# Optimization experiments

Hardware: AMD Instinct MI355X
Metric: run time of the kernel (lower is better)

## Reference

```python
import jax, jax.numpy as jnp
import numpy as np
import math

B, C_IN, S, E, H, DFF = 8, 16, 1024, 128, 8, 512
DH = E // H
EPS_BN = 1e-5
EPS_LN = 1e-5


def _tape_pe(d_model, seq_len):
    pos = jnp.arange(seq_len, dtype=jnp.float32)[:, None]
    div = jnp.exp(jnp.arange(0, d_model, 2, dtype=jnp.float32) * (-math.log(10000.0) / d_model))
    ang = pos * div * (d_model / seq_len)
    pe = jnp.zeros((seq_len, d_model), dtype=jnp.float32)
    pe = pe.at[:, 0::2].set(jnp.sin(ang))
    pe = pe.at[:, 1::2].set(jnp.cos(ang))
    return pe  # [S, E]


def _ln(x, g, b, eps=EPS_LN):
    m = jnp.mean(x, axis=-1, keepdims=True)
    v = jnp.mean((x - m) ** 2, axis=-1, keepdims=True)
    return (x - m) / jnp.sqrt(v + eps) * g + b


def _bn(x, g, b, mean, var, eps=EPS_BN):
    # eval-mode BatchNorm2d over channel axis 1 of NCHW
    sh = (1, -1, 1, 1)
    return (x - mean.reshape(sh)) / jnp.sqrt(var.reshape(sh) + eps) * g.reshape(sh) + b.reshape(sh)


def setup_inputs() -> dict:
    key = jax.random.key(0)
    ks = jax.random.split(key, 24)
    f = lambda k, shape, s=0.05: (jax.random.normal(k, shape, dtype=jnp.float32) * s)
    inp = {
        'x': jax.random.normal(ks[0], (B, C_IN, S), dtype=jnp.float32),
        'conv1_w': f(ks[1], (E * 4, 1, 1, 7)),
        'conv1_b': f(ks[2], (E * 4,)),
        'bn1_g': 1.0 + f(ks[3], (E * 4,)),
        'bn1_b': f(ks[4], (E * 4,)),
        'bn1_m': jnp.zeros((E * 4,), jnp.float32),
        'bn1_v': jnp.ones((E * 4,), jnp.float32),
        'conv2_w': f(ks[5], (E, E * 4, C_IN, 1)),
        'conv2_b': f(ks[6], (E,)),
        'bn2_g': 1.0 + f(ks[7], (E,)),
        'bn2_b': f(ks[8], (E,)),
        'bn2_m': jnp.zeros((E,), jnp.float32),
        'bn2_v': jnp.ones((E,), jnp.float32),
        'wq': f(ks[9], (E, E)),
        'wk': f(ks[10], (E, E)),
        'wv': f(ks[11], (E, E)),
        'rel_bias_table': f(ks[12], (2 * S - 1, H), 0.02),
        'ln_attn_g': jnp.ones((E,), jnp.float32),
        'ln_attn_b': jnp.zeros((E,), jnp.float32),
        'ln1_g': jnp.ones((E,), jnp.float32),
        'ln1_b': jnp.zeros((E,), jnp.float32),
        'ln2_g': jnp.ones((E,), jnp.float32),
        'ln2_b': jnp.zeros((E,), jnp.float32),
        'ff_w1': f(ks[13], (DFF, E)),
        'ff_b1': f(ks[14], (DFF,)),
        'ff_w2': f(ks[15], (E, DFF)),
        'ff_b2': f(ks[16], (E,)),
    }
    return inp


def reference(x, conv1_w, conv1_b, bn1_g, bn1_b, bn1_m, bn1_v,
              conv2_w, conv2_b, bn2_g, bn2_b, bn2_m, bn2_v,
              wq, wk, wv, rel_bias_table,
              ln_attn_g, ln_attn_b, ln1_g, ln1_b, ln2_g, ln2_b,
              ff_w1, ff_b1, ff_w2, ff_b2):
    dn = ('NCHW', 'OIHW', 'NCHW')
    # conv stem: x [B, C_in, S] -> [B, 1, C_in, S]
    h = x[:, None, :, :]
    h = jax.lax.conv_general_dilated(h, conv1_w, (1, 1), [(0, 0), (3, 3)], dimension_numbers=dn)
    h = h + conv1_b[None, :, None, None]
    h = jax.nn.gelu(_bn(h, bn1_g, bn1_b, bn1_m, bn1_v), approximate=False)
    h = jax.lax.conv_general_dilated(h, conv2_w, (1, 1), [(0, 0), (0, 0)], dimension_numbers=dn)
    h = h + conv2_b[None, :, None, None]
    h = jax.nn.gelu(_bn(h, bn2_g, bn2_b, bn2_m, bn2_v), approximate=False)
    x_src = jnp.transpose(h[:, :, 0, :], (0, 2, 1))  # [B, S, E]

    # tAPE absolute positional encoding
    x_pos = x_src + _tape_pe(E, S)[None]

    # Attention_Rel_Scl (eRPE): bias added AFTER softmax, as in the original
    scale = E ** (-0.5)
    q = jnp.einsum('bsd,ed->bse', x_pos, wq).reshape(B, S, H, DH).transpose(0, 2, 1, 3)
    k = jnp.einsum('bsd,ed->bse', x_pos, wk).reshape(B, S, H, DH).transpose(0, 2, 1, 3)
    v = jnp.einsum('bsd,ed->bse', x_pos, wv).reshape(B, S, H, DH).transpose(0, 2, 1, 3)
    attn = jax.nn.softmax(jnp.einsum('bhid,bhjd->bhij', q, k) * scale, axis=-1)
    idx = jnp.arange(S)[:, None] - jnp.arange(S)[None, :] + (S - 1)  # [S, S]
    rel_bias = rel_bias_table[idx].transpose(2, 0, 1)[None]  # [1, H, S, S]
    attn = attn + rel_bias
    out = jnp.einsum('bhij,bhjd->bhid', attn, v).transpose(0, 2, 1, 3).reshape(B, S, E)
    out = _ln(out, ln_attn_g, ln_attn_b)

    att = _ln(x_src + out, ln1_g, ln1_b)
    ff = jnp.maximum(jnp.einsum('bsd,fd->bsf', att, ff_w1) + ff_b1, 0.0)
    ff = jnp.einsum('bsf,ef->bse', ff, ff_w2) + ff_b2
    y = _ln(att + ff, ln2_g, ln2_b)
    return jnp.transpose(y, (0, 2, 1))  # [B, E, S]
```

## Files before the change

kernel.cpp:

```cpp
#include <hip/hip_runtime.h>
#include <math.h>

#define BB    8
#define CIN   16
#define SS    1024
#define EE    128
#define HH    8
#define DHH   16
#define O1    512
#define DFFN  512
#define K2TOT 8192

#define PE_OFF    0
#define BN1SC_OFF 131072
#define BN1SH_OFF 131584
#define BN2SC_OFF 132096
#define BN2SH_OFF 132224
#define W1P_OFF   133120
#define WQKV_BF_OFF 135168
#define W1FF_BF_OFF 159744
#define W2FF_BF_OFF 192512
#define XSRC_OFF  262144
#define Q_OFF     1310720
#define KK_OFF    2359296
#define V_OFF     3407872
#define ATTN_OFF  4456448
#define ATT_OFF   5505024
#define FFH_OFF   6553600
#define W2CONV_BF_OFF 8650752

typedef __attribute__((ext_vector_type(8))) short short8;
typedef __attribute__((ext_vector_type(8))) unsigned short ushort8;
typedef __attribute__((ext_vector_type(4))) unsigned short us4;
typedef __attribute__((ext_vector_type(4))) float f32x4;
typedef _Float16 f16_t;
typedef __attribute__((ext_vector_type(4))) _Float16 half4;
typedef __attribute__((ext_vector_type(8))) _Float16 half8;

__device__ __forceinline__ float wave_sum(float v) {
    #pragma unroll
    for (int o = 32; o > 0; o >>= 1) v += __shfl_xor(v, o);
    return v;
}

__device__ __forceinline__ float gelu_exact(float x) {
    return 0.5f * x * (1.0f + erff(x * 0.7071067811865476f));
}

__device__ __forceinline__ float gelu_tanh(float x) {
    float x2 = x * x;
    float y = x * fmaf(0.0713548162f, x2, 1.5957691216f);
    float E = __expf(y);
    float r = __builtin_amdgcn_rcpf(E + 1.0f);
    return fmaf(-x, r, x);
}

__device__ __forceinline__ unsigned short f2bf(float f) {
    unsigned int u = __float_as_uint(f);
    unsigned int r = u + 0x7FFFu + ((u >> 16) & 1u);
    return (unsigned short)(r >> 16);
}

__device__ __forceinline__ float bf2f(unsigned short u) {
    return __uint_as_float(((unsigned int)u) << 16);
}

__device__ __forceinline__ void castw_body(const float* __restrict__ src,
                                           unsigned short* __restrict__ dst, int K, int tid) {
    int g = tid & 7, e = (tid >> 3) & 127, rest = tid >> 10;
    int KB = K >> 6;
    int kb = rest % KB, nb = rest / KB;
    int col = nb * 128 + e;
    const float* s = src + (size_t)col * K + kb * 64 + ((g ^ (e & 7)) << 3);
    ushort8 v;
    #pragma unroll
    for (int j = 0; j < 8; j++) v[j] = f2bf(s[j]);
    *(ushort8*)&dst[(size_t)tid << 3] = v;
}

__global__ __launch_bounds__(256) void k0_all(const float* __restrict__ conv1_w,
                                              const float* __restrict__ conv1_b,
                                              const float* __restrict__ bn1_g,
                                              const float* __restrict__ bn1_b,
                                              const float* __restrict__ bn1_m,
                                              const float* __restrict__ bn1_v,
                                              const float* __restrict__ conv2_w,
                                              const float* __restrict__ conv2_b,
                                              const float* __restrict__ bn2_g,
                                              const float* __restrict__ bn2_b,
                                              const float* __restrict__ bn2_m,
                                              const float* __restrict__ bn2_v,
                                              const float* __restrict__ wq,
                                              const float* __restrict__ wk,
                                              const float* __restrict__ wv,
                                              const float* __restrict__ ff_w1,
                                              const float* __restrict__ ff_w2,
                                              float* __restrict__ ws) {
    int bid = blockIdx.x, t = threadIdx.x;
    if (bid < 512) {
        int idx = bid * 256 + t;
        int s = idx >> 7, e = idx & 127;
        int i = e >> 1;
        float freq = expf((float)(2 * i) * (-9.210340371976184f / 128.0f));
        float ang = (float)s * freq * 0.125f;
        ws[PE_OFF + idx] = (e & 1) ? cosf(ang) : sinf(ang);
    } else if (bid < 515) {
        int u = (bid - 512) * 256 + t;
        if (u < 512) {
            float sc = bn1_g[u] * rsqrtf(bn1_v[u] + 1e-5f);
            ws[BN1SC_OFF + u] = sc;
            ws[BN1SH_OFF + u] = (conv1_b[u] - bn1_m[u]) * sc + bn1_b[u];
        } else if (u < 640) {
            int e = u - 512;
            float sc = bn2_g[e] * rsqrtf(bn2_v[e] + 1e-5f);
            ws[BN2SC_OFF + e] = sc;
            ws[BN2SH_OFF + e] = (conv2_b[e] - bn2_m[e]) * sc + bn2_b[e];
        }
    } else if (bid < 1027) {
        castw_body(conv2_w, (unsigned short*)(ws + W2CONV_BF_OFF), 8192, (bid - 515) * 256 + t);
    } else if (bid < 1035) {
        castw_body(wq, (unsigned short*)(ws + WQKV_BF_OFF), 128, (bid - 1027) * 256 + t);
    } else if (bid < 1043) {
        castw_body(wk, (unsigned short*)(ws + WQKV_BF_OFF) + 16384, 128, (bid - 1035) * 256 + t);
    } else if (bid < 1051) {
        castw_body(wv, (unsigned short*)(ws + WQKV_BF_OFF) + 32768, 128, (bid - 1043) * 256 + t);
    } else if (bid < 1083) {
        castw_body(ff_w1, (unsigned short*)(ws + W1FF_BF_OFF), 128, (bid - 1051) * 256 + t);
    } else if (bid < 1115) {
        castw_body(ff_w2, (unsigned short*)(ws + W2FF_BF_OFF), 512, (bid - 1083) * 256 + t);
    } else {
        unsigned short* w1p = (unsigned short*)(ws + W1P_OFF);
        for (int id = t; id < 4096; id += 256) {
            int o = id >> 3, u = id & 7;
            float sc = bn1_g[o] * rsqrtf(bn1_v[o] + 1e-5f);
            float v = (u < 7) ? conv1_w[o * 7 + u] * sc : 0.f;
            w1p[id] = f2bf(v);
        }
    }
}

__global__ __launch_bounds__(256) void k1_mfma(const float* __restrict__ x,
                                               float* __restrict__ ws) {
    __shared__ float xt[CIN][24];
    __shared__ unsigned short w1ps[256 * 8];
    __shared__ float sh1s[256];
    __shared__ unsigned short Ab[2][16 * 64];
    __shared__ unsigned short Bbuf[2][128 * 64];

    const int t = threadIdx.x;
    const int wave = t >> 6, lane = t & 63;
    const int row0 = blockIdx.x * 16;
    const int ks = blockIdx.y;
    const int b = row0 >> 10, s0 = row0 & 1023;
    const int obase = ks * 256;

    for (int i = t; i < CIN * 22; i += 256) {
        int c = i / 22, j = i % 22;
        int gs = s0 + j - 3;
        xt[c][j] = (gs >= 0 && gs < SS) ? x[(b * CIN + c) * SS + gs] : 0.f;
    }
    {
        const ushort8* w1pg = (const ushort8*)((const unsigned short*)(ws + W1P_OFF)) + obase;
        for (int i = t; i < 256; i += 256) *(ushort8*)&w1ps[i << 3] = w1pg[i];
        for (int i = t; i < 256; i += 256) sh1s[i] = ws[BN1SH_OFF + obase + i];
    }

    const char* w2g = (const char*)(ws + W2CONV_BF_OFF);

    auto stageB = [&](int kbl, int buf) {
        const char* g = w2g + ((size_t)(ks * 64 + kbl) << 14);
        #pragma unroll
        for (int c4 = 0; c4 < 4; ++c4) {
            int off = c4 * 4096 + wave * 1024;
            __builtin_amdgcn_global_load_lds(
                (const __attribute__((address_space(1))) unsigned int*)(g + off + lane * 16),
                (__attribute__((address_space(3))) unsigned int*)(&Bbuf[buf][off >> 1]),
                16, 0, 0);
        }
    };

    stageB(0, 0);
    __syncthreads();

    const int c_ = lane & 15;
    float xv[10];
    #pragma unroll
    for (int j = 0; j < 10; j++) xv[j] = xt[c_][(wave << 2) + j];
    int wbase[4];
    #pragma unroll
    for (int i = 0; i < 4; i++) {
        int ss = (wave << 2) + i;
        wbase[i] = (ss << 6) + ((((lane >> 3) ^ (ss & 7))) << 3) + (lane & 7);
    }
    unsigned short* abf = &Ab[0][0];

    auto computeH1 = [&](int kbl, int buf) {
        int ol = (kbl << 2) + (lane >> 4);
        ushort8 wv8 = *(const ushort8*)&w1ps[ol << 3];
        float w0 = bf2f(wv8[0]), w1_ = bf2f(wv8[1]), w2_ = bf2f(wv8[2]), w3 = bf2f(wv8[3]);
        float w4 = bf2f(wv8[4]), w5 = bf2f(wv8[5]), w6 = bf2f(wv8[6]);
        float sh = sh1s[ol];
        int boff = buf << 10;
        #pragma unroll
        for (int i = 0; i < 4; i++) {
            float p = xv[i]   * w0 + xv[i+1] * w1_ + xv[i+2] * w2_ + xv[i+3] * w3
                    + xv[i+4] * w4 + xv[i+5] * w5 + xv[i+6] * w6;
            abf[boff + wbase[i]] = f2bf(gelu_tanh(p + sh));
        }
    };

    const int lrow = lane & 15, lq = lane >> 4;
    f32x4 acc[2];
    acc[0] = (f32x4){0.f, 0.f, 0.f, 0.f};
    acc[1] = (f32x4){0.f, 0.f, 0.f, 0.f};

    auto mfmaPhase = [&](int buf) {
        #pragma unroll
        for (int ksname = 0; ksname < 2; ++ksname) {
            int G = (ksname << 2) + lq;
            short8 a = *(const short8*)&Ab[buf][(lrow << 6) + ((G ^ (lrow & 7)) << 3)];
            #pragma unroll
            for (int nf = 0; nf < 2; ++nf) {
                int e = (wave << 5) + (nf << 4) + lrow;
                short8 bf = *(const short8*)&Bbuf[buf][(e << 6) + ((G ^ (e & 7)) << 3)];
                acc[nf] = __builtin_amdgcn_mfma_f32_16x16x32_bf16(a, bf, acc[nf], 0, 0, 0);
            }
        }
    };

    computeH1(0, 0);
    __syncthreads();
    for (int kbl = 0; kbl < 64; ++kbl) {
        int cur = kbl & 1;
        if (kbl < 63) stageB(kbl + 1, cur ^ 1);
        mfmaPhase(cur);
        if (kbl < 63) computeH1(kbl + 1, cur ^ 1);
        __syncthreads();
    }

    float* P = ws + FFH_OFF + (size_t)ks * 1048576;
    #pragma unroll
    for (int nf = 0; nf < 2; ++nf) {
        int e = (wave << 5) + (nf << 4) + lrow;
        #pragma unroll
        for (int r = 0; r < 4; ++r) {
            int srow = s0 + (lq << 2) + r;
            P[(((size_t)(b * SS + srow)) << 7) + e] = acc[nf][r];
        }
    }
}

__global__ __launch_bounds__(256) void k1b_combine(float* __restrict__ ws) {
    int f = (blockIdx.x * 256 + threadIdx.x) * 4;
    int e0 = f & 127;
    float4 p0 = *(const float4*)&ws[FFH_OFF + f];
    float4 p1 = *(const float4*)&ws[FFH_OFF + 1048576 + f];
    float4 sc = *(const float4*)&ws[BN2SC_OFF + e0];
    float4 sh = *(const float4*)&ws[BN2SH_OFF + e0];
    float4 o;
    o.x = gelu_exact(fmaf(p0.x + p1.x, sc.x, sh.x));
    o.y = gelu_exact(fmaf(p0.y + p1.y, sc.y, sh.y));
    o.z = gelu_exact(fmaf(p0.z + p1.z, sc.z, sh.z));
    o.w = gelu_exact(fmaf(p0.w + p1.w, sc.w, sh.w));
    *(float4*)&ws[XSRC_OFF + f] = o;
}

__global__ __launch_bounds__(256) void k2_mfma(float* __restrict__ ws) {
    __shared__ unsigned short As[32 * 128];
    __shared__ unsigned short Bs[128 * 128];
    __shared__ float ys[32][132];
    const int t = threadIdx.x;
    const int rt = blockIdx.x, mat = blockIdx.y;
    const int wave = t >> 6, lane = t & 63;

    const char* bg = (const char*)((const unsigned short*)(ws + WQKV_BF_OFF) + mat * 16384);
    #pragma unroll
    for (int c8 = 0; c8 < 8; ++c8) {
        int off = c8 * 4096 + wave * 1024;
        __builtin_amdgcn_global_load_lds(
            (const __attribute__((address_space(1))) unsigned int*)(bg + off + lane * 16),
            (__attribute__((address_space(3))) unsigned int*)(&Bs[off >> 1]), 16, 0, 0);
    }
    const int bs0 = rt * 32;
    const int sl0 = bs0 & 1023;
    for (int i = t; i < 1024; i += 256) {
        int row = i >> 5, d0 = (i & 31) << 2;
        float4 xvv = *(const float4*)&ws[XSRC_OFF + (size_t)(bs0 + row) * EE + d0];
        float4 pv = *(const float4*)&ws[PE_OFF + (size_t)(sl0 + row) * EE + d0];
        us4 o;
        o[0] = f2bf(xvv.x + pv.x); o[1] = f2bf(xvv.y + pv.y);
        o[2] = f2bf(xvv.z + pv.z); o[3] = f2bf(xvv.w + pv.w);
        int slot = (d0 >> 3) ^ (row & 7);
        *(us4*)&As[(row << 7) + (slot << 3) + (d0 & 7)] = o;
    }
    __syncthreads();

    const int wr = wave >> 1, wc = wave & 1;
    const int lrow = lane & 15, lq = lane >> 4;
    f32x4 acc[4];
    #pragma unroll
    for (int i = 0; i < 4; i++) acc[i] = (f32x4){0.f, 0.f, 0.f, 0.f};

    #pragma unroll
    for (int ksname = 0; ksname < 4; ++ksname) {
        int G = (ksname << 2) + lq;
        int arow = (wr << 4) + lrow;
        short8 a = *(const short8*)&As[(arow << 7) + ((G ^ (arow & 7)) << 3)];
        #pragma unroll
        for (int nf = 0; nf < 4; ++nf) {
            int e = (wc << 6) + (nf << 4) + lrow;
            short8 bf = *(const short8*)&Bs[((G >> 3) << 13) + (e << 6) + (((G & 7) ^ (e & 7)) << 3)];
            acc[nf] = __builtin_amdgcn_mfma_f32_16x16x32_bf16(a, bf, acc[nf], 0, 0, 0);
        }
    }

    #pragma unroll
    for (int nf = 0; nf < 4; ++nf) {
        int e = (wc << 6) + (nf << 4) + lrow;
        #pragma unroll
        for (int r = 0; r < 4; ++r)
            ys[(wr << 4) + (lq << 2) + r][e] = acc[nf][r];
    }
    __syncthreads();

    const int b = bs0 >> 10;
    if (mat <= 1) {
        int row = t >> 3, h8 = t & 7;
        float scl = (mat == 0) ? 0.08838834764831845f : 1.0f;
        f16_t* dst = (f16_t*)(ws + (mat == 0 ? Q_OFF : KK_OFF))
                   + (((size_t)(b * HH + h8)) * SS + (sl0 + row)) * DHH;
        half8 v0, v1;
        #pragma unroll
        for (int d = 0; d < 8; d++) v0[d] = (f16_t)(ys[row][h8 * 16 + d] * scl);
        #pragma unroll
        for (int d = 0; d < 8; d++) v1[d] = (f16_t)(ys[row][h8 * 16 + 8 + d] * scl);
        *(half8*)&dst[0] = v0;
        *(half8*)&dst[8] = v1;
    } else {
        int c = t & 127, hf = t >> 7;
        int h8 = c >> 4, d2 = c & 15;
        f16_t* dst = (f16_t*)(ws + V_OFF)
                   + (((size_t)(b * HH + h8)) * DHH + d2) * SS + sl0 + hf * 16;
        half8 v0, v1;
        #pragma unroll
        for (int r = 0; r < 8; r++) v0[r] = (f16_t)ys[hf * 16 + r][c];
        #pragma unroll
        for (int r = 0; r < 8; r++) v1[r] = (f16_t)ys[hf * 16 + 8 + r][c];
        *(half8*)&dst[0] = v0;
        *(half8*)&dst[8] = v1;
    }
}

__global__ __launch_bounds__(256) void k3_attn(const float* __restrict__ rel_tab,
                                               float* __restrict__ ws) {
    __shared__ f16_t rtbl4[4][1088];
    const int bh = blockIdx.x;
    const int h = bh & 7, b = bh >> 3;
    const int i0b = blockIdx.y * 64;
    const int t = threadIdx.x;
    for (int id = t; id < 4 * 1088; id += 256) {
        int p = id >> 10;
        p = id / 1088; int j = id - p * 1088;
        int u = j + p;
        float v = (u < 1087) ? rel_tab[(i0b + 1086 - u) * HH + h] : 0.f;
        rtbl4[p][j] = (f16_t)v;
    }
    __syncthreads();

    const int w = t >> 6, lane = t & 63;
    const int q = lane & 15, g = lane >> 4;
    const int r = w * 16 + q;
    const int i = i0b + r;

    const f16_t* QH  = (const f16_t*)(ws + Q_OFF)  + (size_t)bh * SS * DHH;
    const f16_t* KH  = (const f16_t*)(ws + KK_OFF) + (size_t)bh * SS * DHH;
    const f16_t* VHT = (const f16_t*)(ws + V_OFF)  + (size_t)bh * DHH * SS;

    half4 qf = *(const half4*)&QH[(size_t)i * DHH + 4 * g];
    f32x4 o = {0.f, 0.f, 0.f, 0.f};
    f32x4 bv = {0.f, 0.f, 0.f, 0.f};
    const f32x4 zf = {0.f, 0.f, 0.f, 0.f};
    float lp = 0.f;
    const int p4 = (63 - r + 4 * g) & 3;

    #pragma unroll 4
    for (int jt = 0; jt < 64; ++jt) {
        half4 kf = *(const half4*)&KH[(size_t)(jt * 16 + q) * DHH + 4 * g];
        f32x4 s = __builtin_amdgcn_mfma_f32_16x16x16f16(kf, qf, zf, 0, 0, 0);
        float p0 = __expf(s[0]), p1 = __expf(s[1]), p2 = __expf(s[2]), p3 = __expf(s[3]);
        lp += (p0 + p1) + (p2 + p3);
        half4 pf;
        pf[0] = (f16_t)p0; pf[1] = (f16_t)p1; pf[2] = (f16_t)p2; pf[3] = (f16_t)p3;
        half4 vf = *(const half4*)&VHT[(size_t)q * SS + jt * 16 + 4 * g];
        o = __builtin_amdgcn_mfma_f32_16x16x16f16(vf, pf, o, 0, 0, 0);
        int vb = 63 - r + jt * 16 + 4 * g;
        half4 bfrag = *(const half4*)&rtbl4[p4][vb & ~3];
        bv = __builtin_amdgcn_mfma_f32_16x16x16f16(vf, bfrag, bv, 0, 0, 0);
    }
    lp += __shfl_xor(lp, 16);
    lp += __shfl_xor(lp, 32);
    float inv = 1.f / lp;
    float4 ov = make_float4(fmaf(o[0], inv, bv[0]), fmaf(o[1], inv, bv[1]),
                            fmaf(o[2], inv, bv[2]), fmaf(o[3], inv, bv[3]));
    *(float4*)&ws[ATTN_OFF + ((size_t)(b * SS) + i) * EE + h * DHH + 4 * g] = ov;
}

__global__ __launch_bounds__(256) void k4_ln(const float* __restrict__ g_attn, const float* __restrict__ b_attn,
                                             const float* __restrict__ g1, const float* __restrict__ b1,
                                             float* __restrict__ ws) {
    int row = blockIdx.x * 4 + (threadIdx.x >> 6);
    int lane = threadIdx.x & 63;
    int e0 = lane * 2;
    const float* ain = ws + ATTN_OFF + (size_t)row * EE;
    const float* xsr = ws + XSRC_OFF + (size_t)row * EE;
    float2 a = *(const float2*)(ain + e0);
    float mean = wave_sum(a.x + a.y) * (1.f / 128.f);
    float dx = a.x - mean, dy = a.y - mean;
    float var = wave_sum(dx * dx + dy * dy) * (1.f / 128.f);
    float inv = rsqrtf(var + 1e-5f);
    float n0 = dx * inv * g_attn[e0] + b_attn[e0];
    float n1 = dy * inv * g_attn[e0 + 1] + b_attn[e0 + 1];
    float2 xs2 = *(const float2*)(xsr + e0);
    float z0 = xs2.x + n0, z1 = xs2.y + n1;
    float m2 = wave_sum(z0 + z1) * (1.f / 128.f);
    float d0 = z0 - m2, d1 = z1 - m2;
    float v2 = wave_sum(d0 * d0 + d1 * d1) * (1.f / 128.f);
    float inv2 = rsqrtf(v2 + 1e-5f);
    float o0 = d0 * inv2 * g1[e0] + b1[e0];
    float o1 = d1 * inv2 * g1[e0 + 1] + b1[e0 + 1];
    *(float2*)(ws + ATT_OFF + (size_t)row * EE + e0) = make_float2(o0, o1);
}

__global__ __launch_bounds__(256) void k5_mfma(const float* __restrict__ b1,
                                               float* __restrict__ ws) {
    __shared__ unsigned short As[32 * 128];
    __shared__ unsigned short Bs[128 * 128];
    __shared__ float ys[32][132];
    const int t = threadIdx.x;
    const int rt = blockIdx.x, nb = blockIdx.y;
    const int wave = t >> 6, lane = t & 63;

    const char* bg = (const char*)((const unsigned short*)(ws + W1FF_BF_OFF) + nb * 16384);
    #pragma unroll
    for (int c8 = 0; c8 < 8; ++c8) {
        int off = c8 * 4096 + wave * 1024;
        __builtin_amdgcn_global_load_lds(
            (const __attribute__((address_space(1))) unsigned int*)(bg + off + lane * 16),
            (__attribute__((address_space(3))) unsigned int*)(&Bs[off >> 1]), 16, 0, 0);
    }
    const int bs0 = rt * 32;
    for (int i = t; i < 1024; i += 256) {
        int row = i >> 5, d0 = (i & 31) << 2;
        float4 xvv = *(const float4*)&ws[ATT_OFF + (size_t)(bs0 + row) * EE + d0];
        us4 o;
        o[0] = f2bf(xvv.x); o[1] = f2bf(xvv.y); o[2] = f2bf(xvv.z); o[3] = f2bf(xvv.w);
        int slot = (d0 >> 3) ^ (row & 7);
        *(us4*)&As[(row << 7) + (slot << 3) + (d0 & 7)] = o;
    }
    __syncthreads();

    const int wr = wave >> 1, wc = wave & 1;
    const int lrow = lane & 15, lq = lane >> 4;
    f32x4 acc[4];
    #pragma unroll
    for (int i = 0; i < 4; i++) acc[i] = (f32x4){0.f, 0.f, 0.f, 0.f};

    #pragma unroll
    for (int ksname = 0; ksname < 4; ++ksname) {
        int G = (ksname << 2) + lq;
        int arow = (wr << 4) + lrow;
        short8 a = *(const short8*)&As[(arow << 7) + ((G ^ (arow & 7)) << 3)];
        #pragma unroll
        for (int nf = 0; nf < 4; ++nf) {
            int e = (wc << 6) + (nf << 4) + lrow;
            short8 bf = *(const short8*)&Bs[((G >> 3) << 13) + (e << 6) + (((G & 7) ^ (e & 7)) << 3)];
            acc[nf] = __builtin_amdgcn_mfma_f32_16x16x32_bf16(a, bf, acc[nf], 0, 0, 0);
        }
    }

    #pragma unroll
    for (int nf = 0; nf < 4; ++nf) {
        int col = (wc << 6) + (nf << 4) + lrow;
        float bias = b1[(nb << 7) + col];
        #pragma unroll
        for (int r = 0; r < 4; ++r)
            ys[(wr << 4) + (lq << 2) + r][col] = fmaxf(acc[nf][r] + bias, 0.f);
    }
    __syncthreads();

    unsigned short* ffhb = (unsigned short*)(ws + FFH_OFF);
    #pragma unroll
    for (int kk = 0; kk < 2; ++kk) {
        int id = t + kk * 256;
        int ssr = id >> 4, fg = id & 15;
        float4 v0 = *(const float4*)&ys[ssr][fg * 8];
        float4 v1 = *(const float4*)&ys[ssr][fg * 8 + 4];
        ushort8 ov;
        ov[0] = f2bf(v0.x); ov[1] = f2bf(v0.y); ov[2] = f2bf(v0.z); ov[3] = f2bf(v0.w);
        ov[4] = f2bf(v1.x); ov[5] = f2bf(v1.y); ov[6] = f2bf(v1.z); ov[7] = f2bf(v1.w);
        int kb = (nb << 1) + (fg >> 3);
        int slot = (fg & 7) ^ (ssr & 7);
        *(ushort8*)&ffhb[(((size_t)(rt * 8 + kb) * 32 + ssr) << 6) + (slot << 3)] = ov;
    }
}

__global__ __launch_bounds__(256) void k6_mfma(const float* __restrict__ b2,
                                               const float* __restrict__ g2, const float* __restrict__ bb2,
                                               float* __restrict__ ws, float* __restrict__ out) {
    __shared__ unsigned short Ab[2][2048];
    __shared__ unsigned short Bb[2][8192];
    __shared__ float y[32][132];
    const int t = threadIdx.x;
    const int wave = t >> 6, lane = t & 63;
    const int rt = blockIdx.x;

    const char* ag = (const char*)((const unsigned short*)(ws + FFH_OFF) + (size_t)rt * 16384);
    const char* bgc = (const char*)(ws + W2FF_BF_OFF);

    auto stage = [&](int kb, int buf) {
        __builtin_amdgcn_global_load_lds(
            (const __attribute__((address_space(1))) unsigned int*)(ag + kb * 4096 + t * 16),
            (__attribute__((address_space(3))) unsigned int*)(&Ab[buf][(t * 16) >> 1]), 16, 0, 0);
        const char* g = bgc + kb * 16384;
        #pragma unroll
        for (int c4 = 0; c4 < 4; ++c4) {
            int off = c4 * 4096 + wave * 1024;
            __builtin_amdgcn_global_load_lds(
                (const __attribute__((address_space(1))) unsigned int*)(g + off + lane * 16),
                (__attribute__((address_space(3))) unsigned int*)(&Bb[buf][off >> 1]), 16, 0, 0);
        }
    };

    const int wr = wave >> 1, wc = wave & 1;
    const int lrow = lane & 15, lq = lane >> 4;
    f32x4 acc[4];
    #pragma unroll
    for (int i = 0; i < 4; i++) acc[i] = (f32x4){0.f, 0.f, 0.f, 0.f};

    stage(0, 0);
    __syncthreads();
    for (int kb = 0; kb < 8; ++kb) {
        int cur = kb & 1;
        if (kb < 7) stage(kb + 1, cur ^ 1);
        #pragma unroll
        for (int ksname = 0; ksname < 2; ++ksname) {
            int G = (ksname << 2) + lq;
            int arow = (wr << 4) + lrow;
            short8 a = *(const short8*)&Ab[cur][(arow << 6) + ((G ^ (arow & 7)) << 3)];
            #pragma unroll
            for (int nf = 0; nf < 4; ++nf) {
                int e = (wc << 6) + (nf << 4) + lrow;
                short8 bf = *(const short8*)&Bb[cur][(e << 6) + ((G ^ (e & 7)) << 3)];
                acc[nf] = __builtin_amdgcn_mfma_f32_16x16x32_bf16(a, bf, acc[nf], 0, 0, 0);
            }
        }
        __syncthreads();
    }

    const int bs0 = rt * 32;
    #pragma unroll
    for (int nf = 0; nf < 4; ++nf) {
        int e = (wc << 6) + (nf << 4) + lrow;
        float bvv = b2[e];
        #pragma unroll
        for (int r = 0; r < 4; ++r) {
            int row = (wr << 4) + (lq << 2) + r;
            y[row][e] = acc[nf][r] + bvv + ws[ATT_OFF + (size_t)(bs0 + row) * EE + e];
        }
    }
    __syncthreads();
    int e0 = lane * 2;
    for (int rr = 0; rr < 8; rr++) {
        int row = wave * 8 + rr;
        float z0 = y[row][e0], z1 = y[row][e0 + 1];
        float mean = wave_sum(z0 + z1) * (1.f / 128.f);
        float d0 = z0 - mean, d1 = z1 - mean;
        float var = wave_sum(d0 * d0 + d1 * d1) * (1.f / 128.f);
        float inv = rsqrtf(var + 1e-5f);
        y[row][e0]     = d0 * inv * g2[e0] + bb2[e0];
        y[row][e0 + 1] = d1 * inv * g2[e0 + 1] + bb2[e0 + 1];
    }
    __syncthreads();
    int b = bs0 >> 10, s0 = bs0 & 1023;
    int sl = t & 31, eg = t >> 5;
    #pragma unroll
    for (int rep = 0; rep < 16; rep++) {
        int e = eg * 16 + rep;
        out[(size_t)b * EE * SS + (size_t)e * SS + s0 + sl] = y[sl][e];
    }
}

extern "C" void kernel_launch(void* const* d_in, const int* in_sizes, int n_in,
                              void* d_out, int out_size, void* d_ws, size_t ws_size,
                              hipStream_t stream) {
    const float* x        = (const float*)d_in[0];
    const float* conv1_w  = (const float*)d_in[1];
    const float* conv1_b  = (const float*)d_in[2];
    const float* bn1_g    = (const float*)d_in[3];
    const float* bn1_b    = (const float*)d_in[4];
    const float* bn1_m    = (const float*)d_in[5];
    const float* bn1_v    = (const float*)d_in[6];
    const float* conv2_w  = (const float*)d_in[7];
    const float* conv2_b  = (const float*)d_in[8];
    const float* bn2_g    = (const float*)d_in[9];
    const float* bn2_b    = (const float*)d_in[10];
    const float* bn2_m    = (const float*)d_in[11];
    const float* bn2_v    = (const float*)d_in[12];
    const float* wq       = (const float*)d_in[13];
    const float* wk       = (const float*)d_in[14];
    const float* wv       = (const float*)d_in[15];
    const float* rel_tab  = (const float*)d_in[16];
    const float* ln_attn_g = (const float*)d_in[17];
    const float* ln_attn_b = (const float*)d_in[18];
    const float* ln1_g    = (const float*)d_in[19];
    const float* ln1_b    = (const float*)d_in[20];
    const float* ln2_g    = (const float*)d_in[21];
    const float* ln2_b    = (const float*)d_in[22];
    const float* ff_w1    = (const float*)d_in[23];
    const float* ff_b1    = (const float*)d_in[24];
    const float* ff_w2    = (const float*)d_in[25];
    const float* ff_b2    = (const float*)d_in[26];

    float* ws  = (float*)d_ws;
    float* out = (float*)d_out;

    hipLaunchKernelGGL(k0_all, dim3(1116), dim3(256), 0, stream,
                       conv1_w, conv1_b, bn1_g, bn1_b, bn1_m, bn1_v,
                       conv2_w, conv2_b, bn2_g, bn2_b, bn2_m, bn2_v,
                       wq, wk, wv, ff_w1, ff_w2, ws);
    hipLaunchKernelGGL(k1_mfma, dim3(512, 2), dim3(256), 0, stream, x, ws);
    hipLaunchKernelGGL(k1b_combine, dim3(1024), dim3(256), 0, stream, ws);
    hipLaunchKernelGGL(k2_mfma, dim3(256, 3), dim3(256), 0, stream, ws);
    hipLaunchKernelGGL(k3_attn, dim3(BB * HH, SS / 64), dim3(256), 0, stream, rel_tab, ws);
    hipLaunchKernelGGL(k4_ln, dim3(BB * SS / 4), dim3(256), 0, stream, ln_attn_g, ln_attn_b, ln1_g, ln1_b, ws);
    hipLaunchKernelGGL(k5_mfma, dim3(256, 4), dim3(256), 0, stream, ff_b1, ws);
    hipLaunchKernelGGL(k6_mfma, dim3(256), dim3(256), 0, stream, ff_b2, ln2_g, ln2_b, ws, out);
}
```

Before: 186.1 us.

## Double k1 row tile and load conv2 weights straight into registers

The conv1+conv2 MFMA kernel now processes 32 rows per block instead of 16, using a 2x2 wave layout where each wave computes 16 rows by 64 columns. This halves the number of blocks, and each conv2 weight tile is reused across twice as many rows. The LDS staging of the B operand through global_load_lds is dropped. Each wave instead loads its B fragments directly from global memory into registers, double-buffered across iterations, with launch bounds set for 3 blocks per SM. In exchange it uses more registers and issues uncached-pattern global loads that are duplicated between the two row-waves, and the grid is smaller.

```diff
diff --git a/kernel.cpp b/kernel.cpp
--- a/kernel.cpp
+++ b/kernel.cpp
@@ -139,60 +139,64 @@
     }
 }
 
-__global__ __launch_bounds__(256) void k1_mfma(const float* __restrict__ x,
-                                               float* __restrict__ ws) {
-    __shared__ float xt[CIN][24];
+__global__ __launch_bounds__(256, 3) void k1_mfma(const float* __restrict__ x,
+                                                  float* __restrict__ ws) {
+    __shared__ float xt[CIN][40];
     __shared__ unsigned short w1ps[256 * 8];
     __shared__ float sh1s[256];
-    __shared__ unsigned short Ab[2][16 * 64];
-    __shared__ unsigned short Bbuf[2][128 * 64];
+    __shared__ unsigned short Ab[2][32 * 64];
 
     const int t = threadIdx.x;
     const int wave = t >> 6, lane = t & 63;
-    const int row0 = blockIdx.x * 16;
-    const int ks = blockIdx.y;
+    const int row0 = blockIdx.x * 32;
+    const int ksplit = blockIdx.y;
     const int b = row0 >> 10, s0 = row0 & 1023;
-    const int obase = ks * 256;
-
-    for (int i = t; i < CIN * 22; i += 256) {
-        int c = i / 22, j = i % 22;
+    const int obase = ksplit * 256;
+
+    for (int i = t; i < CIN * 38; i += 256) {
+        int c = i / 38, j = i % 38;
         int gs = s0 + j - 3;
         xt[c][j] = (gs >= 0 && gs < SS) ? x[(b * CIN + c) * SS + gs] : 0.f;
     }
     {
         const ushort8* w1pg = (const ushort8*)((const unsigned short*)(ws + W1P_OFF)) + obase;
-        for (int i = t; i < 256; i += 256) *(ushort8*)&w1ps[i << 3] = w1pg[i];
-        for (int i = t; i < 256; i += 256) sh1s[i] = ws[BN1SH_OFF + obase + i];
-    }
+        if (t < 256) *(ushort8*)&w1ps[t << 3] = w1pg[t];
+        if (t < 256) sh1s[t] = ws[BN1SH_OFF + obase + t];
+    }
+    __syncthreads();
 
     const char* w2g = (const char*)(ws + W2CONV_BF_OFF);
-
-    auto stageB = [&](int kbl, int buf) {
-        const char* g = w2g + ((size_t)(ks * 64 + kbl) << 14);
-        #pragma unroll
-        for (int c4 = 0; c4 < 4; ++c4) {
-            int off = c4 * 4096 + wave * 1024;
-            __builtin_amdgcn_global_load_lds(
-                (const __attribute__((address_space(1))) unsigned int*)(g + off + lane * 16),
-                (__attribute__((address_space(3))) unsigned int*)(&Bbuf[buf][off >> 1]),
-                16, 0, 0);
-        }
+    const int wr = wave >> 1, wc = wave & 1;
+    const int lrow = lane & 15, lq = lane >> 4;
+
+    int boff[8];
+    #pragma unroll
+    for (int ks2 = 0; ks2 < 2; ++ks2) {
+        int G = (ks2 << 2) + lq;
+        #pragma unroll
+        for (int nf = 0; nf < 4; ++nf) {
+            int e = (wc << 6) + (nf << 4) + lrow;
+            boff[ks2 * 4 + nf] = (e << 7) + ((G ^ (e & 7)) << 4);
+        }
+    }
+
+    auto loadB = [&](int kbl, short8 (&dst)[8]) {
+        const char* g = w2g + ((size_t)(ksplit * 64 + kbl) << 14);
+        #pragma unroll
+        for (int i = 0; i < 8; ++i)
+            dst[i] = *(const short8*)(g + boff[i]);
     };
 
-    stageB(0, 0);
-    __syncthreads();
-
     const int c_ = lane & 15;
-    float xv[10];
-    #pragma unroll
-    for (int j = 0; j < 10; j++) xv[j] = xt[c_][(wave << 2) + j];
-    int wbase[4];
-    #pragma unroll
-    for (int i = 0; i < 4; i++) {
-        int ss = (wave << 2) + i;
+    float xv[14];
+    #pragma unroll
+    for (int j = 0; j < 14; j++) xv[j] = xt[c_][(wave << 3) + j];
+    int wbase[8];
+    #pragma unroll
+    for (int i = 0; i < 8; i++) {
+        int ss = (wave << 3) + i;
         wbase[i] = (ss << 6) + ((((lane >> 3) ^ (ss & 7))) << 3) + (lane & 7);
     }
-    unsigned short* abf = &Ab[0][0];
 
     auto computeH1 = [&](int kbl, int buf) {
         int ol = (kbl << 2) + (lane >> 4);
@@ -200,51 +204,55 @@
         float w0 = bf2f(wv8[0]), w1_ = bf2f(wv8[1]), w2_ = bf2f(wv8[2]), w3 = bf2f(wv8[3]);
         float w4 = bf2f(wv8[4]), w5 = bf2f(wv8[5]), w6 = bf2f(wv8[6]);
         float sh = sh1s[ol];
-        int boff = buf << 10;
-        #pragma unroll
-        for (int i = 0; i < 4; i++) {
+        unsigned short* abf = &Ab[buf][0];
+        #pragma unroll
+        for (int i = 0; i < 8; i++) {
             float p = xv[i]   * w0 + xv[i+1] * w1_ + xv[i+2] * w2_ + xv[i+3] * w3
                     + xv[i+4] * w4 + xv[i+5] * w5 + xv[i+6] * w6;
-            abf[boff + wbase[i]] = f2bf(gelu_tanh(p + sh));
+            abf[wbase[i]] = f2bf(gelu_tanh(p + sh));
         }
     };
 
-    const int lrow = lane & 15, lq = lane >> 4;
-    f32x4 acc[2];
-    acc[0] = (f32x4){0.f, 0.f, 0.f, 0.f};
-    acc[1] = (f32x4){0.f, 0.f, 0.f, 0.f};
-
-    auto mfmaPhase = [&](int buf) {
-        #pragma unroll
-        for (int ksname = 0; ksname < 2; ++ksname) {
-            int G = (ksname << 2) + lq;
-            short8 a = *(const short8*)&Ab[buf][(lrow << 6) + ((G ^ (lrow & 7)) << 3)];
+    f32x4 acc[4];
+    #pragma unroll
+    for (int i = 0; i < 4; i++) acc[i] = (f32x4){0.f, 0.f, 0.f, 0.f};
+
+    auto mfmaPhase = [&](short8 (&bb)[8], int buf) {
+        #pragma unroll
+        for (int ks2 = 0; ks2 < 2; ++ks2) {
+            int G = (ks2 << 2) + lq;
+            int arow = (wr << 4) + lrow;
+            short8 a = *(const short8*)&Ab[buf][(arow << 6) + ((G ^ (arow & 7)) << 3)];
             #pragma unroll
-            for (int nf = 0; nf < 2; ++nf) {
-                int e = (wave << 5) + (nf << 4) + lrow;
-                short8 bf = *(const short8*)&Bbuf[buf][(e << 6) + ((G ^ (e & 7)) << 3)];
-                acc[nf] = __builtin_amdgcn_mfma_f32_16x16x32_bf16(a, bf, acc[nf], 0, 0, 0);
-            }
+            for (int nf = 0; nf < 4; ++nf)
+                acc[nf] = __builtin_amdgcn_mfma_f32_16x16x32_bf16(a, bb[ks2 * 4 + nf], acc[nf], 0, 0, 0);
         }
     };
 
+    short8 bA[8], bB[8];
+    loadB(0, bA);
     computeH1(0, 0);
     __syncthreads();
-    for (int kbl = 0; kbl < 64; ++kbl) {
-        int cur = kbl & 1;
-        if (kbl < 63) stageB(kbl + 1, cur ^ 1);
-        mfmaPhase(cur);
-        if (kbl < 63) computeH1(kbl + 1, cur ^ 1);
+    for (int kb2 = 0; kb2 < 64; kb2 += 2) {
+        loadB(kb2 + 1, bB);
+        mfmaPhase(bA, 0);
+        computeH1(kb2 + 1, 1);
         __syncthreads();
-    }
-
-    float* P = ws + FFH_OFF + (size_t)ks * 1048576;
-    #pragma unroll
-    for (int nf = 0; nf < 2; ++nf) {
-        int e = (wave << 5) + (nf << 4) + lrow;
+        if (kb2 + 2 < 64) loadB(kb2 + 2, bA);
+        mfmaPhase(bB, 1);
+        if (kb2 + 2 < 64) {
+            computeH1(kb2 + 2, 0);
+            __syncthreads();
+        }
+    }
+
+    float* P = ws + FFH_OFF + (size_t)ksplit * 1048576;
+    #pragma unroll
+    for (int nf = 0; nf < 4; ++nf) {
+        int e = (wc << 6) + (nf << 4) + lrow;
         #pragma unroll
         for (int r = 0; r < 4; ++r) {
-            int srow = s0 + (lq << 2) + r;
+            int srow = s0 + (wr << 4) + (lq << 2) + r;
             P[(((size_t)(b * SS + srow)) << 7) + e] = acc[nf][r];
         }
     }
@@ -359,8 +367,7 @@
     const int i0b = blockIdx.y * 64;
     const int t = threadIdx.x;
     for (int id = t; id < 4 * 1088; id += 256) {
-        int p = id >> 10;
-        p = id / 1088; int j = id - p * 1088;
+        int p = id / 1088; int j = id - p * 1088;
         int u = j + p;
         float v = (u < 1087) ? rel_tab[(i0b + 1086 - u) * HH + h] : 0.f;
         rtbl4[p][j] = (f16_t)v;
@@ -628,7 +635,7 @@
                        conv1_w, conv1_b, bn1_g, bn1_b, bn1_m, bn1_v,
                        conv2_w, conv2_b, bn2_g, bn2_b, bn2_m, bn2_v,
                        wq, wk, wv, ff_w1, ff_w2, ws);
-    hipLaunchKernelGGL(k1_mfma, dim3(512, 2), dim3(256), 0, stream, x, ws);
+    hipLaunchKernelGGL(k1_mfma, dim3(256, 2), dim3(256), 0, stream, x, ws);
     hipLaunchKernelGGL(k1b_combine, dim3(1024), dim3(256), 0, stream, ws);
     hipLaunchKernelGGL(k2_mfma, dim3(256, 3), dim3(256), 0, stream, ws);
     hipLaunchKernelGGL(k3_attn, dim3(BB * HH, SS / 64), dim3(256), 0, stream, rel_tab, ws);
```

Result: faster. 168.0 us (-9.7%).
